# Optimization experiments

Measured on AMD Instinct MI355X. Metric: run time of the kernel, lower is better.

Reference implementation:

```python
import jax, jax.numpy as jnp
import numpy as np

DT = 1.0  # module init dt

def setup_inputs() -> dict:
    key = jax.random.key(0)
    k1, k2 = jax.random.split(key)
    x = jax.random.normal(k1, (8, 4096, 512), dtype=jnp.float32)
    w = jax.random.normal(k2, (512,), dtype=jnp.float32)
    return {"x": x, "w": w}

def reference(x, w):
    # h_t = h_{t-1} + dt*(x_t - relu(w)*h_{t-1}) = a*h_{t-1} + dt*x_t,  a = 1 - dt*relu(w)
    a = (1.0 - DT * jax.nn.relu(w)).astype(x.dtype)  # [d]
    h0 = jnp.zeros((x.shape[0], x.shape[2]), dtype=x.dtype)  # [b, d]
    xt = jnp.swapaxes(x, 0, 1)  # [t, b, d]

    def step(h, x_t):
        h_next = a * h + DT * x_t
        return h_next, h_next

    _, hs = jax.lax.scan(step, h0, xt)  # [t, b, d]
    return jnp.swapaxes(hs, 0, 1)  # [b, t, d] (return_sequences=True)
```

## Files before the change

### kernel.cpp

```cpp
#include <hip/hip_runtime.h>


#define RB 8
#define RT 4096
#define RD 512
#define DG (RD / 4)
#define CL 16
#define NC (RT / CL)
#define TPB 1024
#define HB 1e15f

typedef float f32x4 __attribute__((ext_vector_type(4)));

__device__ __forceinline__ float sclamp(float v) {
    return fminf(fmaxf(v, -HB), HB);
}
__device__ __forceinline__ f32x4 sclamp4(f32x4 v) {
    v.x = sclamp(v.x); v.y = sclamp(v.y);
    v.z = sclamp(v.z); v.w = sclamp(v.w);
    return v;
}
__device__ __forceinline__ f32x4 ld4(const float4* __restrict__ p) {
    return *(const f32x4* __restrict__)p;
}
__device__ __forceinline__ f32x4 shfl4(f32x4 v, int src) {
    f32x4 r;
    r.x = __shfl(v.x, src, 64);
    r.y = __shfl(v.y, src, 64);
    r.z = __shfl(v.z, src, 64);
    r.w = __shfl(v.w, src, 64);
    return r;
}
__device__ __forceinline__ f32x4 relu_decay(float4 wq) {
    f32x4 a;
    a.x = 1.0f - fmaxf(wq.x, 0.0f);
    a.y = 1.0f - fmaxf(wq.y, 0.0f);
    a.z = 1.0f - fmaxf(wq.z, 0.0f);
    a.w = 1.0f - fmaxf(wq.w, 0.0f);
    return a;
}

__global__ void __launch_bounds__(TPB, 4)
rnn_fused(const float4* __restrict__ x4, const float4* __restrict__ w4,
          float4* __restrict__ out4) {
    const int tid = threadIdx.x;
    const int g   = tid & 3;
    const int c   = tid >> 2;

    const int bid  = blockIdx.x;
    const int u    = bid & 7;
    const int half = (bid >> 3) & 1;
    const int rest = bid >> 4;
    const int pair = rest * 8 + u;
    const int b    = pair >> 4;
    const int tile = 2 * (pair & 15) + half;

    const f32x4 A1 = relu_decay(w4[tile * 4 + g]);

    __shared__ f32x4 Wagg[NC * 5];
    __shared__ f32x4 CI[NC * 5];
    __shared__ f32x4 WinAgg[4 * 5];

    const size_t base = ((size_t)b * RT + (size_t)c * CL) * DG
                      + (size_t)(tile * 4 + g);
    const float4* __restrict__ xb = x4 + base;

    f32x4 hl[CL];
#pragma unroll
    for (int i = 0; i < CL; ++i) hl[i] = ld4(xb + (size_t)i * DG);
    {
        f32x4 h = {0.f, 0.f, 0.f, 0.f};
#pragma unroll
        for (int i = 0; i < CL; ++i) {
            h = sclamp4(A1 * h + hl[i]);
            hl[i] = h;
        }
        Wagg[c * 5 + g] = h;
    }
    __syncthreads();

    {
        const int w  = tid >> 6;
        const int l  = tid & 63;
        const int g2 = w & 3;
        const int q  = w >> 2;
        const int cc = q * 64 + l;

        f32x4 B = relu_decay(w4[tile * 4 + g2]);
#pragma unroll
        for (int i = 0; i < 4; ++i) B = sclamp4(B * B);

        f32x4 S = Wagg[cc * 5 + g2];
        f32x4 M = B;
#pragma unroll
        for (int s = 1; s < 64; s <<= 1) {
            f32x4 t = shfl4(S, l >= s ? l - s : l);
            S = (l >= s) ? sclamp4(M * t + S) : S;
            M = sclamp4(M * M);
        }
        if (l == 63) WinAgg[q * 5 + g2] = S;
        __syncthreads();

        f32x4 WC = {0.f, 0.f, 0.f, 0.f};
#pragma unroll
        for (int j = 0; j < 3; ++j) {
            if (j < q) WC = sclamp4(M * WC + WinAgg[j * 5 + g2]);
        }
        const int n = l + 1;
        f32x4 P = {1.f, 1.f, 1.f, 1.f};
        f32x4 mm = B;
#pragma unroll
        for (int k = 0; k < 7; ++k) {
            if ((n >> k) & 1) P = sclamp4(P * mm);
            mm = sclamp4(mm * mm);
        }
        f32x4 Sf = sclamp4(S + P * WC);
        if (cc < NC - 1) CI[(cc + 1) * 5 + g2] = Sf;
        if (cc == 0)     CI[0 * 5 + g2] = (f32x4){0.f, 0.f, 0.f, 0.f};
    }
    __syncthreads();

    {
        float4* __restrict__ ob = out4 + base;
        const f32x4 C = CI[c * 5 + g];
        f32x4 p = A1;
#pragma unroll
        for (int i = 0; i < CL; ++i) {
            f32x4 o = sclamp4(hl[i] + p * C);
            __builtin_nontemporal_store(o, (f32x4*)(ob + (size_t)i * DG));
            p = sclamp4(p * A1);
        }
    }
}

extern "C" void kernel_launch(void* const* d_in, const int* in_sizes, int n_in,
                              void* d_out, int out_size, void* d_ws, size_t ws_size,
                              hipStream_t stream) {
    const float4* x4 = (const float4*)d_in[0];
    const float4* w4 = (const float4*)d_in[1];
    float4* o4 = (float4*)d_out;
    rnn_fused<<<dim3(RB * (RD / 16)), dim3(TPB), 0, stream>>>(x4, w4, o4);
}
```

Before: 118.4 us.

## Recompute chunk scan from reloaded input instead of holding chunk in registers

Stop keeping the 16 per-chunk partial states in registers across the cross-chunk scan phase. The first pass streams x with a 4-deep software prefetch and keeps only the running state. The final pass reloads x and reruns the local recurrence seeded with the chunk carry-in. This cuts register pressure and may raise occupancy, at the cost of reading x twice from memory or cache.

```diff
diff --git a/kernel.cpp b/kernel.cpp
--- a/kernel.cpp
+++ b/kernel.cpp
@@ -41,8 +41,8 @@
 }
 
 __global__ void __launch_bounds__(TPB, 4)
-rnn_fused(const float4* __restrict__ x4, const float4* __restrict__ w4,
-          float4* __restrict__ out4) {
+rnn_fused2(const float4* __restrict__ x4, const float4* __restrict__ w4,
+           float4* __restrict__ out4) {
     const int tid = threadIdx.x;
     const int g   = tid & 3;
     const int c   = tid >> 2;
@@ -65,16 +65,28 @@
                       + (size_t)(tile * 4 + g);
     const float4* __restrict__ xb = x4 + base;
 
-    f32x4 hl[CL];
-#pragma unroll
-    for (int i = 0; i < CL; ++i) hl[i] = ld4(xb + (size_t)i * DG);
     {
         f32x4 h = {0.f, 0.f, 0.f, 0.f};
-#pragma unroll
-        for (int i = 0; i < CL; ++i) {
-            h = sclamp4(A1 * h + hl[i]);
-            hl[i] = h;
-        }
+        f32x4 v0 = ld4(xb + 0 * DG), v1 = ld4(xb + 1 * DG);
+        f32x4 v2 = ld4(xb + 2 * DG), v3 = ld4(xb + 3 * DG);
+#define CONSUME4()                                   \
+        h = sclamp4(A1 * h + v0);                    \
+        h = sclamp4(A1 * h + v1);                    \
+        h = sclamp4(A1 * h + v2);                    \
+        h = sclamp4(A1 * h + v3);
+#define PREFETCH4(B)                                 \
+        { f32x4 n0 = ld4(xb + (size_t)((B) + 0) * DG);   \
+          f32x4 n1 = ld4(xb + (size_t)((B) + 1) * DG);   \
+          f32x4 n2 = ld4(xb + (size_t)((B) + 2) * DG);   \
+          f32x4 n3 = ld4(xb + (size_t)((B) + 3) * DG);   \
+          CONSUME4();                                \
+          v0 = n0; v1 = n1; v2 = n2; v3 = n3; }
+        PREFETCH4(4)
+        PREFETCH4(8)
+        PREFETCH4(12)
+        CONSUME4()
+#undef PREFETCH4
+#undef CONSUME4
         Wagg[c * 5 + g] = h;
     }
     __syncthreads();
@@ -122,14 +134,31 @@
 
     {
         float4* __restrict__ ob = out4 + base;
-        const f32x4 C = CI[c * 5 + g];
-        f32x4 p = A1;
-#pragma unroll
-        for (int i = 0; i < CL; ++i) {
-            f32x4 o = sclamp4(hl[i] + p * C);
-            __builtin_nontemporal_store(o, (f32x4*)(ob + (size_t)i * DG));
-            p = sclamp4(p * A1);
-        }
+        f32x4 h = CI[c * 5 + g];
+        f32x4 v0 = ld4(xb + 0 * DG), v1 = ld4(xb + 1 * DG);
+        f32x4 v2 = ld4(xb + 2 * DG), v3 = ld4(xb + 3 * DG);
+#define CONSUME4S(B)                                                     \
+        h = sclamp4(A1 * h + v0);                                        \
+        __builtin_nontemporal_store(h, (f32x4*)(ob + (size_t)((B)+0)*DG)); \
+        h = sclamp4(A1 * h + v1);                                        \
+        __builtin_nontemporal_store(h, (f32x4*)(ob + (size_t)((B)+1)*DG)); \
+        h = sclamp4(A1 * h + v2);                                        \
+        __builtin_nontemporal_store(h, (f32x4*)(ob + (size_t)((B)+2)*DG)); \
+        h = sclamp4(A1 * h + v3);                                        \
+        __builtin_nontemporal_store(h, (f32x4*)(ob + (size_t)((B)+3)*DG));
+#define PREFETCH4S(B)                                \
+        { f32x4 n0 = ld4(xb + (size_t)((B) + 4) * DG);   \
+          f32x4 n1 = ld4(xb + (size_t)((B) + 5) * DG);   \
+          f32x4 n2 = ld4(xb + (size_t)((B) + 6) * DG);   \
+          f32x4 n3 = ld4(xb + (size_t)((B) + 7) * DG);   \
+          CONSUME4S(B);                              \
+          v0 = n0; v1 = n1; v2 = n2; v3 = n3; }
+        PREFETCH4S(0)
+        PREFETCH4S(4)
+        PREFETCH4S(8)
+        CONSUME4S(12)
+#undef PREFETCH4S
+#undef CONSUME4S
     }
 }
 
@@ -139,5 +168,5 @@
     const float4* x4 = (const float4*)d_in[0];
     const float4* w4 = (const float4*)d_in[1];
     float4* o4 = (float4*)d_out;
-    rnn_fused<<<dim3(RB * (RD / 16)), dim3(TPB), 0, stream>>>(x4, w4, o4);
+    rnn_fused2<<<dim3(RB * (RD / 16)), dim3(TPB), 0, stream>>>(x4, w4, o4);
 }
```

Result: slower. 131.4 us (+11.0%).

## Widen feature tile, lengthen chunks, and recompute scan by re-reading x

Applied to the files above, without the earlier changes.

Each block now covers 8 float4 feature groups and 32 timesteps per thread, giving 128 chunks per block and two scan windows instead of four. The kernel no longer holds the whole chunk in registers between phases. It streams x with a 4-deep software prefetch in the local pass, then re-reads x after the cross-chunk scan and recomputes the recurrence from the carried-in state while storing outputs. This lowers register pressure and halves the block count, but it reads x twice from global memory, likely served from L2. The block-index swizzle is also dropped in favour of a direct batch/tile mapping.

```diff
diff --git a/kernel.cpp b/kernel.cpp
--- a/kernel.cpp
+++ b/kernel.cpp
@@ -5,9 +5,12 @@
 #define RT 4096
 #define RD 512
 #define DG (RD / 4)
-#define CL 16
+#define TG 8
+#define NTL (DG / TG)
+#define CL 32
 #define NC (RT / CL)
 #define TPB 1024
+#define PF 4
 #define HB 1e15f
 
 typedef float f32x4 __attribute__((ext_vector_type(4)));
@@ -41,56 +44,62 @@
 }
 
 __global__ void __launch_bounds__(TPB, 4)
-rnn_fused(const float4* __restrict__ x4, const float4* __restrict__ w4,
-          float4* __restrict__ out4) {
+rnn_fused3(const float4* __restrict__ x4, const float4* __restrict__ w4,
+           float4* __restrict__ out4) {
     const int tid = threadIdx.x;
-    const int g   = tid & 3;
-    const int c   = tid >> 2;
+    const int g   = tid & (TG - 1);
+    const int c   = tid >> 3;
 
     const int bid  = blockIdx.x;
-    const int u    = bid & 7;
-    const int half = (bid >> 3) & 1;
-    const int rest = bid >> 4;
-    const int pair = rest * 8 + u;
-    const int b    = pair >> 4;
-    const int tile = 2 * (pair & 15) + half;
+    const int b    = bid >> 4;
+    const int tile = bid & (NTL - 1);
 
-    const f32x4 A1 = relu_decay(w4[tile * 4 + g]);
+    const f32x4 A1 = relu_decay(w4[tile * TG + g]);
 
-    __shared__ f32x4 Wagg[NC * 5];
-    __shared__ f32x4 CI[NC * 5];
-    __shared__ f32x4 WinAgg[4 * 5];
+    __shared__ f32x4 Wagg[NC * 9];
+    __shared__ f32x4 CI[NC * 9];
+    __shared__ f32x4 WinAgg[2 * 9];
 
     const size_t base = ((size_t)b * RT + (size_t)c * CL) * DG
-                      + (size_t)(tile * 4 + g);
+                      + (size_t)(tile * TG + g);
     const float4* __restrict__ xb = x4 + base;
 
-    f32x4 hl[CL];
+    {
+        f32x4 v[PF];
 #pragma unroll
-    for (int i = 0; i < CL; ++i) hl[i] = ld4(xb + (size_t)i * DG);
-    {
+        for (int k = 0; k < PF; ++k) v[k] = ld4(xb + (size_t)k * DG);
         f32x4 h = {0.f, 0.f, 0.f, 0.f};
 #pragma unroll
-        for (int i = 0; i < CL; ++i) {
-            h = sclamp4(A1 * h + hl[i]);
-            hl[i] = h;
+        for (int bb = 0; bb < CL; bb += PF) {
+            f32x4 n[PF];
+            if (bb + PF < CL) {
+#pragma unroll
+                for (int k = 0; k < PF; ++k)
+                    n[k] = ld4(xb + (size_t)(bb + PF + k) * DG);
+            }
+#pragma unroll
+            for (int k = 0; k < PF; ++k) h = sclamp4(A1 * h + v[k]);
+            if (bb + PF < CL) {
+#pragma unroll
+                for (int k = 0; k < PF; ++k) v[k] = n[k];
+            }
         }
-        Wagg[c * 5 + g] = h;
+        Wagg[c * 9 + g] = h;
     }
     __syncthreads();
 
     {
         const int w  = tid >> 6;
         const int l  = tid & 63;
-        const int g2 = w & 3;
-        const int q  = w >> 2;
+        const int g2 = w & (TG - 1);
+        const int q  = w >> 3;
         const int cc = q * 64 + l;
 
-        f32x4 B = relu_decay(w4[tile * 4 + g2]);
+        f32x4 B = relu_decay(w4[tile * TG + g2]);
 #pragma unroll
-        for (int i = 0; i < 4; ++i) B = sclamp4(B * B);
+        for (int i = 0; i < 5; ++i) B = sclamp4(B * B);
 
-        f32x4 S = Wagg[cc * 5 + g2];
+        f32x4 S = Wagg[cc * 9 + g2];
         f32x4 M = B;
 #pragma unroll
         for (int s = 1; s < 64; s <<= 1) {
@@ -98,14 +107,11 @@
             S = (l >= s) ? sclamp4(M * t + S) : S;
             M = sclamp4(M * M);
         }
-        if (l == 63) WinAgg[q * 5 + g2] = S;
+        if (l == 63) WinAgg[q * 9 + g2] = S;
         __syncthreads();
 
         f32x4 WC = {0.f, 0.f, 0.f, 0.f};
-#pragma unroll
-        for (int j = 0; j < 3; ++j) {
-            if (j < q) WC = sclamp4(M * WC + WinAgg[j * 5 + g2]);
-        }
+        if (q == 1) WC = WinAgg[0 * 9 + g2];
         const int n = l + 1;
         f32x4 P = {1.f, 1.f, 1.f, 1.f};
         f32x4 mm = B;
@@ -115,20 +121,35 @@
             mm = sclamp4(mm * mm);
         }
         f32x4 Sf = sclamp4(S + P * WC);
-        if (cc < NC - 1) CI[(cc + 1) * 5 + g2] = Sf;
-        if (cc == 0)     CI[0 * 5 + g2] = (f32x4){0.f, 0.f, 0.f, 0.f};
+        if (cc < NC - 1) CI[(cc + 1) * 9 + g2] = Sf;
+        if (cc == 0)     CI[0 * 9 + g2] = (f32x4){0.f, 0.f, 0.f, 0.f};
     }
     __syncthreads();
 
     {
         float4* __restrict__ ob = out4 + base;
-        const f32x4 C = CI[c * 5 + g];
-        f32x4 p = A1;
+        f32x4 h = CI[c * 9 + g];
+        f32x4 v[PF];
 #pragma unroll
-        for (int i = 0; i < CL; ++i) {
-            f32x4 o = sclamp4(hl[i] + p * C);
-            __builtin_nontemporal_store(o, (f32x4*)(ob + (size_t)i * DG));
-            p = sclamp4(p * A1);
+        for (int k = 0; k < PF; ++k) v[k] = ld4(xb + (size_t)k * DG);
+#pragma unroll
+        for (int bb = 0; bb < CL; bb += PF) {
+            f32x4 n[PF];
+            if (bb + PF < CL) {
+#pragma unroll
+                for (int k = 0; k < PF; ++k)
+                    n[k] = ld4(xb + (size_t)(bb + PF + k) * DG);
+            }
+#pragma unroll
+            for (int k = 0; k < PF; ++k) {
+                h = sclamp4(A1 * h + v[k]);
+                __builtin_nontemporal_store(
+                    h, (f32x4*)(ob + (size_t)(bb + k) * DG));
+            }
+            if (bb + PF < CL) {
+#pragma unroll
+                for (int k = 0; k < PF; ++k) v[k] = n[k];
+            }
         }
     }
 }
@@ -139,5 +160,5 @@
     const float4* x4 = (const float4*)d_in[0];
     const float4* w4 = (const float4*)d_in[1];
     float4* o4 = (float4*)d_out;
-    rnn_fused<<<dim3(RB * (RD / 16)), dim3(TPB), 0, stream>>>(x4, w4, o4);
+    rnn_fused3<<<dim3(RB * NTL), dim3(TPB), 0, stream>>>(x4, w4, o4);
 }
```

Measured after the change: 138.9 us. 1.17x slower.
